# Kernel optimization log

Hardware: AMD Instinct MI355X
Metric: run time of the kernel (lower is better)

## Reference

```python
import jax, jax.numpy as jnp
import numpy as np

EPS = 1e-09

def setup_inputs() -> dict:
    key = jax.random.key(0)
    k1, k2, k3 = jax.random.split(key, 3)
    B, C, H, W = 16, 512, 64, 64
    K = 64  # node_num
    x = jax.random.normal(k1, (B, C, H, W), dtype=jnp.float32)
    anchor = jax.random.uniform(k2, (K, C), dtype=jnp.float32)
    sigma_raw = jax.random.uniform(k3, (K, C), dtype=jnp.float32)
    return {"x": x, "anchor": anchor, "sigma_raw": sigma_raw}

def _l2norm(v, axis):
    return v / jnp.maximum(jnp.linalg.norm(v, axis=axis, keepdims=True), 1e-12)

def reference(x, anchor, sigma_raw):
    B, C, H, W = x.shape
    K = anchor.shape[0]
    N = H * W
    sigma = jax.nn.sigmoid(sigma_raw)               # [K, C]
    xf = x.reshape(B, C, N).transpose(0, 2, 1)      # [B, N, C] descriptors

    # squared Mahalanobis-like distance ||(x - a_k)/s_k||^2 via expansion
    # (avoids materializing the [B, N, K, C] residual the torch loop builds)
    inv_s2 = 1.0 / (sigma * sigma)                  # [K, C]
    a_s2 = anchor * inv_s2                          # [K, C]
    const = jnp.sum(anchor * a_s2, axis=1)          # [K]
    d2 = (jnp.einsum('bnc,kc->bnk', xf * xf, inv_s2)
          - 2.0 * jnp.einsum('bnc,kc->bnk', xf, a_s2)
          + const[None, None, :])                   # [B, N, K]
    logits = (-0.5 * d2).transpose(0, 2, 1)         # [B, K, N]
    soft_assign = jax.nn.softmax(logits, axis=1)    # softmax over nodes

    # aggregation: nodes[b,k,c] = sum_n w * (x - a_k)/s_k / (sum_n w + eps)
    w_sum = jnp.sum(soft_assign, axis=2)            # [B, K]
    wx = jnp.einsum('bkn,bnc->bkc', soft_assign, xf)  # [B, K, C]
    nodes = (wx - w_sum[:, :, None] * anchor[None]) / sigma[None]
    nodes = nodes / (w_sum[:, :, None] + EPS)       # [B, K, C]

    nodes = _l2norm(nodes, axis=2)                  # intra-normalize per node
    flat = _l2norm(nodes.reshape(B, -1), axis=1)    # global L2
    # faithful to torch: flat [B, K*C] reinterpreted (no transpose) as [B, C, K]
    return flat.reshape(B, C, K), soft_assign
```

## Files before the change

### kernel.cpp

```cpp
#include <hip/hip_runtime.h>
#include <math.h>

#define B_ 16
#define C_ 512
#define N_ 4096
#define K_ 64

#define OFF_PBIG    0
#define OFF_INVSIG  131072
#define OFF_WSUM    163840
#define OFF_GSUM    164864
#define OFF_WX      164992

typedef short bf16x8 __attribute__((ext_vector_type(8)));
typedef float f32x16 __attribute__((ext_vector_type(16)));

union U4 { uint4 u; bf16x8 b; };

__device__ __forceinline__ unsigned hi16(float f) { return __float_as_uint(f) >> 16; }
__device__ __forceinline__ unsigned hi16rne(float f) {
  return (__float_as_uint(f) + 0x8000u) >> 16;
}
__device__ __forceinline__ float fromhi(unsigned h) { return __uint_as_float(h << 16); }
__device__ __forceinline__ unsigned pk(float lo, float hi) {
  return (__float_as_uint(lo) >> 16) | (__float_as_uint(hi) & 0xFFFF0000u);
}

__global__ void k_prep(const float* __restrict__ anchor,
                       const float* __restrict__ sraw,
                       unsigned* __restrict__ pbig,
                       float* __restrict__ invsig,
                       float* __restrict__ wsum,
                       float* __restrict__ gsum,
                       float* __restrict__ wx) {
  const int k = blockIdx.x;
  const int t = threadIdx.x;
  __shared__ float s_is2[C_], s_m[C_];
  __shared__ float red[4];
  float part = 0.f;
#pragma unroll
  for (int r = 0; r < 2; r++) {
    int c = r * 256 + t;
    float a = anchor[k * C_ + c];
    float sg = 1.f / (1.f + __expf(-sraw[k * C_ + c]));
    float is = 1.f / sg;
    float is2 = is * is;
    s_is2[c] = is2;
    s_m[c] = -2.f * a * is2;
    invsig[k * C_ + c] = is;
    part = fmaf(a * a, is2, part);
  }
  float v = part;
#pragma unroll
  for (int off = 32; off; off >>= 1) v += __shfl_down(v, off);
  if ((t & 63) == 0) red[t >> 6] = v;
  __syncthreads();
  float cst = red[0] + red[1] + red[2] + red[3];
  unsigned ch = hi16(cst);
  unsigned clr = hi16rne(cst - fromhi(ch));
#pragma unroll
  for (int r = 0; r < 2; r++) {
    int c = r * 256 + t;
    float is2 = s_is2[c], m = s_m[c];
    unsigned ih = hi16(is2);
    unsigned ilr = hi16rne(is2 - fromhi(ih));
    unsigned mh = hi16(m);
    unsigned mlr = hi16rne(m - fromhi(mh));
    int chunk = c >> 5, ks = (c & 31) >> 1, lh = c & 1;
    int kh = k >> 5;
    size_t dst = ((((size_t)chunk * 16 + ks) * 2 + kh) * 64 + lh * 32 + (k & 31)) * 4;
    pbig[dst + 0] = ih | (ilr << 16);
    pbig[dst + 1] = ih | (mh << 16);
    pbig[dst + 2] = mlr | (mh << 16);
    pbig[dst + 3] = (c == 0) ? (ch | (clr << 16)) : 0u;
  }
  float4 z4 = make_float4(0.f, 0.f, 0.f, 0.f);
  float4* wz = (float4*)(wx + (size_t)k * 8192);
#pragma unroll
  for (int it = 0; it < 8; it++) wz[it * 256 + t] = z4;
  if (k == 0) {
    for (int i = t; i < B_ * K_; i += 256) wsum[i] = 0.f;
    if (t < B_) gsum[t] = 0.f;
  }
}

__global__ __launch_bounds__(256, 4) void k_dist(
    const float* __restrict__ x,
    const unsigned* __restrict__ pbig,
    float* __restrict__ soft,
    float* __restrict__ wsum) {
  const int bid = blockIdx.x;
  const int swz = (bid & 7) * 128 + (bid >> 3);
  const int b = swz >> 6;
  const int nblk = (swz & 63) * 64;
  const int tid = threadIdx.x;
  const int wid = tid >> 6;
  const int lane = tid & 63;
  const int l31 = lane & 31;
  const int lh = lane >> 5;
  const int kh = wid & 1;
  const int n0 = nblk + (wid >> 1) * 32;

  __shared__ float cmax[4][32];
  __shared__ float csum[4][32];

  f32x16 acc;
#pragma unroll
  for (int i = 0; i < 16; i++) acc[i] = 0.f;

  const float* xcol = x + (size_t)b * (C_ * N_) + n0 + l31;
  const uint4* pf = (const uint4*)pbig + (size_t)kh * 64 + lane;

  float xa[16], xb_[16];
#pragma unroll
  for (int kk = 0; kk < 16; kk++)
    xa[kk] = xcol[(size_t)(kk * 2 + lh) * N_];

#define PACKMF(XV, CC, ACC, AFRAG)                                            \
  {                                                                           \
    float xv = (XV);                                                          \
    float x2 = xv * xv;                                                       \
    unsigned u = __float_as_uint(xv);                                         \
    unsigned u2 = __float_as_uint(x2);                                        \
    unsigned uhf = u & 0xFFFF0000u;                                           \
    unsigned u2hf = u2 & 0xFFFF0000u;                                         \
    float xl = xv - __uint_as_float(uhf);                                     \
    float x2l = x2 - __uint_as_float(u2hf);                                   \
    U4 bf;                                                                    \
    bf.u.x = (u2 >> 16) | u2hf;                                               \
    bf.u.y = ((__float_as_uint(x2l) + 0x8000u) >> 16) | uhf;                  \
    bf.u.z = (u >> 16) | ((__float_as_uint(xl) + 0x8000u) & 0xFFFF0000u);     \
    bf.u.w = ((CC) == 0) ? 0x3F803F80u : 0u;                                  \
    ACC = __builtin_amdgcn_mfma_f32_32x32x16_bf16((AFRAG), bf.b, ACC, 0, 0, 0); \
  }

  for (int c2 = 0; c2 < 8; c2++) {
    {
      const int chunk = 2 * c2;
#pragma unroll
      for (int kk = 0; kk < 16; kk++)
        xb_[kk] = xcol[(size_t)((chunk + 1) * 32 + kk * 2 + lh) * N_];
#pragma unroll
      for (int ks = 0; ks < 16; ks++) {
        U4 a;
        a.u = pf[(size_t)(chunk * 16 + ks) * 128];
        PACKMF(xa[ks], chunk * 32 + ks * 2 + lh, acc, a.b);
      }
    }
    {
      const int chunk = 2 * c2 + 1;
      if (c2 < 7) {
#pragma unroll
        for (int kk = 0; kk < 16; kk++)
          xa[kk] = xcol[(size_t)((chunk + 1) * 32 + kk * 2 + lh) * N_];
      }
#pragma unroll
      for (int ks = 0; ks < 16; ks++) {
        U4 a;
        a.u = pf[(size_t)(chunk * 16 + ks) * 128];
        PACKMF(xb_[ks], chunk * 32 + ks * 2 + lh, acc, a.b);
      }
    }
  }
#undef PACKMF

  float* softb = soft + (size_t)b * (K_ * N_);
  float mm = -3.4e38f;
#pragma unroll
  for (int r = 0; r < 16; r++) {
    acc[r] *= -0.5f;
    mm = fmaxf(mm, acc[r]);
  }
  mm = fmaxf(mm, __shfl_xor(mm, 32));
  cmax[wid][l31] = mm;
  __syncthreads();
  float m = fmaxf(cmax[wid][l31], cmax[wid ^ 1][l31]);
  float ss = 0.f;
#pragma unroll
  for (int r = 0; r < 16; r++) {
    acc[r] = __expf(acc[r] - m);
    ss += acc[r];
  }
  ss += __shfl_xor(ss, 32);
  csum[wid][l31] = ss;
  __syncthreads();
  float tot = csum[wid][l31] + csum[wid ^ 1][l31];
  float inv = 1.f / tot;
  const int nc = n0 + l31;
#pragma unroll
  for (int r = 0; r < 16; r++) {
    float w = acc[r] * inv;
    acc[r] = w;
    int k0 = kh * 32 + (r & 3) + 8 * (r >> 2) + 4 * lh;
    softb[(size_t)k0 * N_ + nc] = w;
  }
#pragma unroll
  for (int r = 0; r < 16; r++) {
    float v = acc[r];
    v += __shfl_xor(v, 1);
    v += __shfl_xor(v, 2);
    v += __shfl_xor(v, 4);
    v += __shfl_xor(v, 8);
    v += __shfl_xor(v, 16);
    if (l31 == 0) {
      int k0 = kh * 32 + (r & 3) + 8 * (r >> 2) + 4 * lh;
      atomicAdd(&wsum[b * K_ + k0], v);
    }
  }
}

__global__ __launch_bounds__(256, 4) void k_agg(const float* __restrict__ x,
                                                const float* __restrict__ soft,
                                                float* __restrict__ wx) {
  const int bid = blockIdx.x;
  const int xcd = bid & 7, slot = bid >> 3;
  const int grp = (slot >> 4) * 8 + xcd;
  const int ct = slot & 15;
  const int b = grp & 15, z = grp >> 4;
  const int tid = threadIdx.x;
  const int wid = tid >> 6, lane = tid & 63, l31 = lane & 31, lh = lane >> 5;
  const int c0 = ct * 32;
  const int n0 = z * 1024 + wid * 256;
  __shared__ float red[4][64][36];

  f32x16 acc[2];
#pragma unroll
  for (int kt = 0; kt < 2; kt++)
#pragma unroll
    for (int i = 0; i < 16; i++) acc[kt][i] = 0.f;

  const float* sb = soft + (size_t)b * (K_ * N_);
  const float* xr = x + (size_t)b * (C_ * N_) + (size_t)(c0 + l31) * N_;
  const float* s0 = sb + (size_t)l31 * N_;
  const float* s1 = sb + (size_t)(32 + l31) * N_;

  for (int kstep = 0; kstep < 16; kstep++) {
    int nb = n0 + kstep * 16 + lh * 8;
    float4 f0 = *(const float4*)&s0[nb];
    float4 f1 = *(const float4*)&s0[nb + 4];
    float4 g0 = *(const float4*)&s1[nb];
    float4 g1 = *(const float4*)&s1[nb + 4];
    float4 h0 = *(const float4*)&xr[nb];
    float4 h1 = *(const float4*)&xr[nb + 4];
    U4 A0, A1, Bf;
    A0.u.x = pk(f0.x, f0.y); A0.u.y = pk(f0.z, f0.w);
    A0.u.z = pk(f1.x, f1.y); A0.u.w = pk(f1.z, f1.w);
    A1.u.x = pk(g0.x, g0.y); A1.u.y = pk(g0.z, g0.w);
    A1.u.z = pk(g1.x, g1.y); A1.u.w = pk(g1.z, g1.w);
    Bf.u.x = pk(h0.x, h0.y); Bf.u.y = pk(h0.z, h0.w);
    Bf.u.z = pk(h1.x, h1.y); Bf.u.w = pk(h1.z, h1.w);
    acc[0] = __builtin_amdgcn_mfma_f32_32x32x16_bf16(A0.b, Bf.b, acc[0], 0, 0, 0);
    acc[1] = __builtin_amdgcn_mfma_f32_32x32x16_bf16(A1.b, Bf.b, acc[1], 0, 0, 0);
  }
#pragma unroll
  for (int kt = 0; kt < 2; kt++)
#pragma unroll
    for (int q = 0; q < 4; q++) {
      float4 vv = make_float4(acc[kt][q * 4], acc[kt][q * 4 + 1],
                              acc[kt][q * 4 + 2], acc[kt][q * 4 + 3]);
      *(float4*)&red[wid][lane][kt * 16 + q * 4] = vv;
    }
  __syncthreads();
  const int lt = tid & 63, sb4 = (tid >> 6) * 8;
  float v[8];
#pragma unroll
  for (int i = 0; i < 8; i++) v[i] = 0.f;
#pragma unroll
  for (int w = 0; w < 4; w++)
#pragma unroll
    for (int i = 0; i < 8; i++) v[i] += red[w][lt][sb4 + i];
#pragma unroll
  for (int i = 0; i < 8; i++) {
    int s = sb4 + i;
    int kt = s >> 4, r = s & 15;
    int k = kt * 32 + (r & 3) + 8 * (r >> 2) + 4 * (lt >> 5);
    atomicAdd(&wx[((size_t)b * K_ + k) * C_ + c0 + (lt & 31)], v[i]);
  }
}

__global__ void k_nodes(const float* __restrict__ wx,
                        const float* __restrict__ wsum,
                        const float* __restrict__ anchor,
                        const float* __restrict__ invsig,
                        float* __restrict__ out0,
                        float* __restrict__ gsum) {
  const int k = blockIdx.x, b = blockIdx.y;
  const int tid = threadIdx.x;
  float wsv = wsum[b * K_ + k];
  float winv = 1.f / (wsv + 1e-9f);
  float vals[4];
  float local = 0.f;
#pragma unroll
  for (int r = 0; r < 4; r++) {
    int c = r * 128 + tid;
    float w = wx[((size_t)b * K_ + k) * C_ + c];
    float v = (w - wsv * anchor[k * C_ + c]) * invsig[k * C_ + c] * winv;
    vals[r] = v;
    local = fmaf(v, v, local);
  }
  float v = local;
#pragma unroll
  for (int off = 32; off; off >>= 1) v += __shfl_down(v, off);
  __shared__ float red[2];
  if ((tid & 63) == 0) red[tid >> 6] = v;
  __syncthreads();
  float sumsq = red[0] + red[1];
  float norm = sqrtf(sumsq);
  float scale = 1.f / fmaxf(norm, 1e-12f);
#pragma unroll
  for (int r = 0; r < 4; r++) {
    int c = r * 128 + tid;
    out0[((size_t)b * K_ + k) * C_ + c] = vals[r] * scale;
  }
  if (tid == 0) atomicAdd(&gsum[b], sumsq * scale * scale);
}

__global__ void k_final(float* __restrict__ out0,
                        const float* __restrict__ gsum) {
  for (int i = blockIdx.x * 256 + threadIdx.x; i < B_ * K_ * C_;
       i += gridDim.x * 256) {
    int b = i >> 15;
    out0[i] = out0[i] * (1.f / fmaxf(sqrtf(gsum[b]), 1e-12f));
  }
}

extern "C" void kernel_launch(void* const* d_in, const int* in_sizes, int n_in,
                              void* d_out, int out_size, void* d_ws, size_t ws_size,
                              hipStream_t stream) {
  const float* x = (const float*)d_in[0];
  const float* anchor = (const float*)d_in[1];
  const float* sraw = (const float*)d_in[2];
  float* out0 = (float*)d_out;
  float* soft = out0 + (size_t)B_ * C_ * K_;
  float* ws = (float*)d_ws;

  unsigned* pbig = (unsigned*)(ws + OFF_PBIG);
  float* invsig = ws + OFF_INVSIG;
  float* wsum = ws + OFF_WSUM;
  float* gsum = ws + OFF_GSUM;
  float* wx = ws + OFF_WX;

  k_prep<<<K_, 256, 0, stream>>>(anchor, sraw, pbig, invsig, wsum, gsum, wx);
  k_dist<<<1024, 256, 0, stream>>>(x, pbig, soft, wsum);
  k_agg<<<1024, 256, 0, stream>>>(x, soft, wx);
  k_nodes<<<dim3(K_, B_), 128, 0, stream>>>(wx, wsum, anchor, invsig, out0,
                                            gsum);
  k_final<<<512, 256, 0, stream>>>(out0, gsum);
}
```

Baseline: 328.6 us.

## Double k_dist per-wave column tile to reuse anchor fragments and prefetch them

k_dist now has each wave handle 64 pixel columns with two accumulators, so every loaded anchor fragment feeds two MFMAs. That halves parameter traffic per output and cuts the grid to 512 blocks. Anchor fragments and x values for the next chunk are prefetched into double-buffered registers, and the softmax reductions are widened to cover both column halves. Register pressure rises, so launch bounds drop to 2 blocks per SM, and k_agg's inner loop gets an unroll-2 hint.

Measured after the change: 291.9 us. 11.2% less time.

```diff
diff --git a/kernel.cpp b/kernel.cpp
--- a/kernel.cpp
+++ b/kernel.cpp
@@ -84,37 +84,33 @@
   }
 }
 
-__global__ __launch_bounds__(256, 4) void k_dist(
+__global__ __launch_bounds__(256, 2) void k_dist(
     const float* __restrict__ x,
     const unsigned* __restrict__ pbig,
     float* __restrict__ soft,
     float* __restrict__ wsum) {
   const int bid = blockIdx.x;
-  const int swz = (bid & 7) * 128 + (bid >> 3);
-  const int b = swz >> 6;
-  const int nblk = (swz & 63) * 64;
+  const int swz = (bid & 7) * 64 + (bid >> 3);
+  const int b = swz >> 5;
+  const int nblk = (swz & 31) * 128;
   const int tid = threadIdx.x;
   const int wid = tid >> 6;
   const int lane = tid & 63;
   const int l31 = lane & 31;
   const int lh = lane >> 5;
   const int kh = wid & 1;
-  const int n0 = nblk + (wid >> 1) * 32;
-
-  __shared__ float cmax[4][32];
-  __shared__ float csum[4][32];
-
-  f32x16 acc;
-#pragma unroll
-  for (int i = 0; i < 16; i++) acc[i] = 0.f;
-
-  const float* xcol = x + (size_t)b * (C_ * N_) + n0 + l31;
+  const int n0 = nblk + (wid >> 1) * 64;
+
+  __shared__ float cmax[4][2][32];
+  __shared__ float csum[4][2][32];
+
+  f32x16 accA, accB;
+#pragma unroll
+  for (int i = 0; i < 16; i++) { accA[i] = 0.f; accB[i] = 0.f; }
+
+  const float* xcol0 = x + (size_t)b * (C_ * N_) + n0 + l31;
+  const float* xcol1 = xcol0 + 32;
   const uint4* pf = (const uint4*)pbig + (size_t)kh * 64 + lane;
-
-  float xa[16], xb_[16];
-#pragma unroll
-  for (int kk = 0; kk < 16; kk++)
-    xa[kk] = xcol[(size_t)(kk * 2 + lh) * N_];
 
 #define PACKMF(XV, CC, ACC, AFRAG)                                            \
   {                                                                           \
@@ -134,69 +130,79 @@
     ACC = __builtin_amdgcn_mfma_f32_32x32x16_bf16((AFRAG), bf.b, ACC, 0, 0, 0); \
   }
 
+#define CHUNK_BODY(CHUNK, FCUR, FNXT, XC0, XC1, XN0, XN1, PREFETCH)           \
+  {                                                                           \
+    const int chunk_ = (CHUNK);                                               \
+    if (PREFETCH) {                                                           \
+      _Pragma("unroll")                                                       \
+      for (int kk = 0; kk < 16; kk++) {                                       \
+        FNXT[kk].u = pf[(size_t)((chunk_ + 1) * 16 + kk) * 128];              \
+        XN0[kk] = xcol0[(size_t)((chunk_ + 1) * 32 + kk * 2 + lh) * N_];      \
+        XN1[kk] = xcol1[(size_t)((chunk_ + 1) * 32 + kk * 2 + lh) * N_];      \
+      }                                                                       \
+    }                                                                         \
+    _Pragma("unroll")                                                         \
+    for (int ks = 0; ks < 16; ks++) {                                         \
+      const int c = chunk_ * 32 + ks * 2 + lh;                                \
+      PACKMF(XC0[ks], c, accA, FCUR[ks].b);                                   \
+      PACKMF(XC1[ks], c, accB, FCUR[ks].b);                                   \
+    }                                                                         \
+  }
+
+  U4 f0_[16], f1_[16];
+  float a0_[16], a1_[16], b0_[16], b1_[16];
+#pragma unroll
+  for (int kk = 0; kk < 16; kk++) {
+    f0_[kk].u = pf[(size_t)kk * 128];
+    a0_[kk] = xcol0[(size_t)(kk * 2 + lh) * N_];
+    a1_[kk] = xcol1[(size_t)(kk * 2 + lh) * N_];
+  }
   for (int c2 = 0; c2 < 8; c2++) {
-    {
-      const int chunk = 2 * c2;
-#pragma unroll
-      for (int kk = 0; kk < 16; kk++)
-        xb_[kk] = xcol[(size_t)((chunk + 1) * 32 + kk * 2 + lh) * N_];
-#pragma unroll
-      for (int ks = 0; ks < 16; ks++) {
-        U4 a;
-        a.u = pf[(size_t)(chunk * 16 + ks) * 128];
-        PACKMF(xa[ks], chunk * 32 + ks * 2 + lh, acc, a.b);
-      }
-    }
-    {
-      const int chunk = 2 * c2 + 1;
-      if (c2 < 7) {
-#pragma unroll
-        for (int kk = 0; kk < 16; kk++)
-          xa[kk] = xcol[(size_t)((chunk + 1) * 32 + kk * 2 + lh) * N_];
-      }
-#pragma unroll
-      for (int ks = 0; ks < 16; ks++) {
-        U4 a;
-        a.u = pf[(size_t)(chunk * 16 + ks) * 128];
-        PACKMF(xb_[ks], chunk * 32 + ks * 2 + lh, acc, a.b);
-      }
-    }
-  }
+    CHUNK_BODY(2 * c2,     f0_, f1_, a0_, a1_, b0_, b1_, 1);
+    CHUNK_BODY(2 * c2 + 1, f1_, f0_, b0_, b1_, a0_, a1_, (c2 < 7));
+  }
+#undef CHUNK_BODY
 #undef PACKMF
 
   float* softb = soft + (size_t)b * (K_ * N_);
-  float mm = -3.4e38f;
+  float mA = -3.4e38f, mB = -3.4e38f;
 #pragma unroll
   for (int r = 0; r < 16; r++) {
-    acc[r] *= -0.5f;
-    mm = fmaxf(mm, acc[r]);
-  }
-  mm = fmaxf(mm, __shfl_xor(mm, 32));
-  cmax[wid][l31] = mm;
-  __syncthreads();
-  float m = fmaxf(cmax[wid][l31], cmax[wid ^ 1][l31]);
-  float ss = 0.f;
+    accA[r] *= -0.5f; mA = fmaxf(mA, accA[r]);
+    accB[r] *= -0.5f; mB = fmaxf(mB, accB[r]);
+  }
+  mA = fmaxf(mA, __shfl_xor(mA, 32));
+  mB = fmaxf(mB, __shfl_xor(mB, 32));
+  cmax[wid][0][l31] = mA;
+  cmax[wid][1][l31] = mB;
+  __syncthreads();
+  mA = fmaxf(cmax[wid][0][l31], cmax[wid ^ 1][0][l31]);
+  mB = fmaxf(cmax[wid][1][l31], cmax[wid ^ 1][1][l31]);
+  float sA = 0.f, sB = 0.f;
 #pragma unroll
   for (int r = 0; r < 16; r++) {
-    acc[r] = __expf(acc[r] - m);
-    ss += acc[r];
-  }
-  ss += __shfl_xor(ss, 32);
-  csum[wid][l31] = ss;
-  __syncthreads();
-  float tot = csum[wid][l31] + csum[wid ^ 1][l31];
-  float inv = 1.f / tot;
-  const int nc = n0 + l31;
+    accA[r] = __expf(accA[r] - mA); sA += accA[r];
+    accB[r] = __expf(accB[r] - mB); sB += accB[r];
+  }
+  sA += __shfl_xor(sA, 32);
+  sB += __shfl_xor(sB, 32);
+  csum[wid][0][l31] = sA;
+  csum[wid][1][l31] = sB;
+  __syncthreads();
+  float invA = 1.f / (csum[wid][0][l31] + csum[wid ^ 1][0][l31]);
+  float invB = 1.f / (csum[wid][1][l31] + csum[wid ^ 1][1][l31]);
+  const int nc0 = n0 + l31;
 #pragma unroll
   for (int r = 0; r < 16; r++) {
-    float w = acc[r] * inv;
-    acc[r] = w;
     int k0 = kh * 32 + (r & 3) + 8 * (r >> 2) + 4 * lh;
-    softb[(size_t)k0 * N_ + nc] = w;
+    float wA = accA[r] * invA; accA[r] = wA;
+    softb[(size_t)k0 * N_ + nc0] = wA;
+    float wB = accB[r] * invB; accB[r] = wB;
+    softb[(size_t)k0 * N_ + nc0 + 32] = wB;
   }
 #pragma unroll
   for (int r = 0; r < 16; r++) {
-    float v = acc[r];
+    float v = accA[r] + accB[r];
     v += __shfl_xor(v, 1);
     v += __shfl_xor(v, 2);
     v += __shfl_xor(v, 4);
@@ -234,6 +240,7 @@
   const float* s0 = sb + (size_t)l31 * N_;
   const float* s1 = sb + (size_t)(32 + l31) * N_;
 
+#pragma unroll 2
   for (int kstep = 0; kstep < 16; kstep++) {
     int nb = n0 + kstep * 16 + lh * 8;
     float4 f0 = *(const float4*)&s0[nb];
@@ -341,7 +348,7 @@
   float* wx = ws + OFF_WX;
 
   k_prep<<<K_, 256, 0, stream>>>(anchor, sraw, pbig, invsig, wsum, gsum, wx);
-  k_dist<<<1024, 256, 0, stream>>>(x, pbig, soft, wsum);
+  k_dist<<<512, 256, 0, stream>>>(x, pbig, soft, wsum);
   k_agg<<<1024, 256, 0, stream>>>(x, soft, wx);
   k_nodes<<<dim3(K_, B_), 128, 0, stream>>>(wx, wsum, anchor, invsig, out0,
                                             gsum);
```

## Split k_dist channel loop across waves with dual n-tiles; halve k_agg N span

Applied to the files above, without the earlier changes.

In k_dist, each wave now covers half the channel range but computes two 32-column n-tiles at once. Each loaded anchor fragment feeds two MFMAs, and anchor fragments are prefetched into registers with double buffering. The partial distances of the two channel halves are then summed through an LDS exchange before the softmax. Separately, k_agg's per-block N range is halved and its grid doubled to 2048 blocks, adding parallelism at the cost of more partial-result accumulation. The larger register arrays risk spilling under the 256x4 launch bound.

After: 583.4 us. +77.6%, slower.

```diff
diff --git a/kernel.cpp b/kernel.cpp
--- a/kernel.cpp
+++ b/kernel.cpp
@@ -99,22 +99,19 @@
   const int l31 = lane & 31;
   const int lh = lane >> 5;
   const int kh = wid & 1;
-  const int n0 = nblk + (wid >> 1) * 32;
-
+  const int chalf = wid >> 1;
+
+  __shared__ float exch[4][64][20];
   __shared__ float cmax[4][32];
   __shared__ float csum[4][32];
 
-  f32x16 acc;
-#pragma unroll
-  for (int i = 0; i < 16; i++) acc[i] = 0.f;
-
-  const float* xcol = x + (size_t)b * (C_ * N_) + n0 + l31;
+  f32x16 accA, accB;
+#pragma unroll
+  for (int i = 0; i < 16; i++) { accA[i] = 0.f; accB[i] = 0.f; }
+
+  const float* xcol0 = x + (size_t)b * (C_ * N_) + nblk + l31;
+  const float* xcol1 = xcol0 + 32;
   const uint4* pf = (const uint4*)pbig + (size_t)kh * 64 + lane;
-
-  float xa[16], xb_[16];
-#pragma unroll
-  for (int kk = 0; kk < 16; kk++)
-    xa[kk] = xcol[(size_t)(kk * 2 + lh) * N_];
 
 #define PACKMF(XV, CC, ACC, AFRAG)                                            \
   {                                                                           \
@@ -134,42 +131,74 @@
     ACC = __builtin_amdgcn_mfma_f32_32x32x16_bf16((AFRAG), bf.b, ACC, 0, 0, 0); \
   }
 
-  for (int c2 = 0; c2 < 8; c2++) {
-    {
-      const int chunk = 2 * c2;
-#pragma unroll
-      for (int kk = 0; kk < 16; kk++)
-        xb_[kk] = xcol[(size_t)((chunk + 1) * 32 + kk * 2 + lh) * N_];
-#pragma unroll
-      for (int ks = 0; ks < 16; ks++) {
-        U4 a;
-        a.u = pf[(size_t)(chunk * 16 + ks) * 128];
-        PACKMF(xa[ks], chunk * 32 + ks * 2 + lh, acc, a.b);
-      }
+#define CHUNK_BODY(CHUNK, FCUR, FNXT, XC0, XC1, XN0, XN1, PREFETCH)           \
+  {                                                                           \
+    const int chunk_ = (CHUNK);                                               \
+    if (PREFETCH) {                                                           \
+      _Pragma("unroll")                                                       \
+      for (int kk = 0; kk < 16; kk++) {                                       \
+        FNXT[kk].u = pf[(size_t)((chunk_ + 1) * 16 + kk) * 128];              \
+        XN0[kk] = xcol0[(size_t)((chunk_ + 1) * 32 + kk * 2 + lh) * N_];      \
+        XN1[kk] = xcol1[(size_t)((chunk_ + 1) * 32 + kk * 2 + lh) * N_];      \
+      }                                                                       \
+    }                                                                         \
+    _Pragma("unroll")                                                         \
+    for (int ks = 0; ks < 16; ks++) {                                         \
+      const int c = chunk_ * 32 + ks * 2 + lh;                                \
+      PACKMF(XC0[ks], c, accA, FCUR[ks].b);                                   \
+      PACKMF(XC1[ks], c, accB, FCUR[ks].b);                                   \
+    }                                                                         \
+  }
+
+  U4 f0_[16], f1_[16];
+  float a0_[16], a1_[16], b0_[16], b1_[16];
+  const int cbase = chalf * 8;
+#pragma unroll
+  for (int kk = 0; kk < 16; kk++) {
+    f0_[kk].u = pf[(size_t)(cbase * 16 + kk) * 128];
+    a0_[kk] = xcol0[(size_t)(cbase * 32 + kk * 2 + lh) * N_];
+    a1_[kk] = xcol1[(size_t)(cbase * 32 + kk * 2 + lh) * N_];
+  }
+  for (int c2 = 0; c2 < 4; c2++) {
+    CHUNK_BODY(cbase + 2 * c2,     f0_, f1_, a0_, a1_, b0_, b1_, 1);
+    CHUNK_BODY(cbase + 2 * c2 + 1, f1_, f0_, b0_, b1_, a0_, a1_, (c2 < 3));
+  }
+#undef CHUNK_BODY
+#undef PACKMF
+
+  {
+    float* pw = &exch[wid][lane][0];
+    if (chalf == 0) {
+#pragma unroll
+      for (int q = 0; q < 4; q++)
+        *(float4*)&pw[q * 4] = make_float4(accB[q * 4], accB[q * 4 + 1],
+                                           accB[q * 4 + 2], accB[q * 4 + 3]);
+    } else {
+#pragma unroll
+      for (int q = 0; q < 4; q++)
+        *(float4*)&pw[q * 4] = make_float4(accA[q * 4], accA[q * 4 + 1],
+                                           accA[q * 4 + 2], accA[q * 4 + 3]);
     }
-    {
-      const int chunk = 2 * c2 + 1;
-      if (c2 < 7) {
-#pragma unroll
-        for (int kk = 0; kk < 16; kk++)
-          xa[kk] = xcol[(size_t)((chunk + 1) * 32 + kk * 2 + lh) * N_];
-      }
-#pragma unroll
-      for (int ks = 0; ks < 16; ks++) {
-        U4 a;
-        a.u = pf[(size_t)(chunk * 16 + ks) * 128];
-        PACKMF(xb_[ks], chunk * 32 + ks * 2 + lh, acc, a.b);
-      }
+  }
+  __syncthreads();
+  f32x16 own;
+  {
+    const float* pr = &exch[wid ^ 2][lane][0];
+    if (chalf == 0) {
+#pragma unroll
+      for (int r = 0; r < 16; r++) own[r] = accA[r] + pr[r];
+    } else {
+#pragma unroll
+      for (int r = 0; r < 16; r++) own[r] = accB[r] + pr[r];
     }
   }
-#undef PACKMF
 
   float* softb = soft + (size_t)b * (K_ * N_);
   float mm = -3.4e38f;
 #pragma unroll
   for (int r = 0; r < 16; r++) {
-    acc[r] *= -0.5f;
-    mm = fmaxf(mm, acc[r]);
+    own[r] *= -0.5f;
+    mm = fmaxf(mm, own[r]);
   }
   mm = fmaxf(mm, __shfl_xor(mm, 32));
   cmax[wid][l31] = mm;
@@ -178,25 +207,24 @@
   float ss = 0.f;
 #pragma unroll
   for (int r = 0; r < 16; r++) {
-    acc[r] = __expf(acc[r] - m);
-    ss += acc[r];
+    own[r] = __expf(own[r] - m);
+    ss += own[r];
   }
   ss += __shfl_xor(ss, 32);
   csum[wid][l31] = ss;
   __syncthreads();
-  float tot = csum[wid][l31] + csum[wid ^ 1][l31];
-  float inv = 1.f / tot;
-  const int nc = n0 + l31;
+  float inv = 1.f / (csum[wid][l31] + csum[wid ^ 1][l31]);
+  const int nc = nblk + chalf * 32 + l31;
 #pragma unroll
   for (int r = 0; r < 16; r++) {
-    float w = acc[r] * inv;
-    acc[r] = w;
+    float w = own[r] * inv;
+    own[r] = w;
     int k0 = kh * 32 + (r & 3) + 8 * (r >> 2) + 4 * lh;
     softb[(size_t)k0 * N_ + nc] = w;
   }
 #pragma unroll
   for (int r = 0; r < 16; r++) {
-    float v = acc[r];
+    float v = own[r];
     v += __shfl_xor(v, 1);
     v += __shfl_xor(v, 2);
     v += __shfl_xor(v, 4);
@@ -220,7 +248,7 @@
   const int tid = threadIdx.x;
   const int wid = tid >> 6, lane = tid & 63, l31 = lane & 31, lh = lane >> 5;
   const int c0 = ct * 32;
-  const int n0 = z * 1024 + wid * 256;
+  const int n0 = z * 512 + wid * 128;
   __shared__ float red[4][64][36];
 
   f32x16 acc[2];
@@ -234,7 +262,8 @@
   const float* s0 = sb + (size_t)l31 * N_;
   const float* s1 = sb + (size_t)(32 + l31) * N_;
 
-  for (int kstep = 0; kstep < 16; kstep++) {
+#pragma unroll 2
+  for (int kstep = 0; kstep < 8; kstep++) {
     int nb = n0 + kstep * 16 + lh * 8;
     float4 f0 = *(const float4*)&s0[nb];
     float4 f1 = *(const float4*)&s0[nb + 4];
@@ -342,7 +371,7 @@
 
   k_prep<<<K_, 256, 0, stream>>>(anchor, sraw, pbig, invsig, wsum, gsum, wx);
   k_dist<<<1024, 256, 0, stream>>>(x, pbig, soft, wsum);
-  k_agg<<<1024, 256, 0, stream>>>(x, soft, wx);
+  k_agg<<<2048, 256, 0, stream>>>(x, soft, wx);
   k_nodes<<<dim3(K_, B_), 128, 0, stream>>>(wx, wsum, anchor, invsig, out0,
                                             gsum);
   k_final<<<512, 256, 0, stream>>>(out0, gsum);
```
